# Kernel tuning notes

Measured on AMD Instinct MI355X. Metric: run time of the kernel, lower is better.

## Reference

```python
import jax, jax.numpy as jnp
import numpy as np

B, T, C, H = 2, 2048, 1024, 16
R = 32
LORA_SCALE = 0.5  # lora_alpha / r = (0.5*rank) / rank
HD = C // H


def setup_inputs() -> dict:
    key = jax.random.key(0)
    ks = jax.random.split(key, 8)
    std = 0.02
    return {
        "x": jax.random.normal(ks[0], (B, T, C), jnp.float32),
        "w_attn": jax.random.normal(ks[1], (3 * C, C), jnp.float32) * std,
        "b_attn": jnp.zeros((3 * C,), jnp.float32),
        "la_attn": jax.random.normal(ks[2], (R, C), jnp.float32) * std,
        "lb_attn": jax.random.normal(ks[3], (3 * C, R), jnp.float32) * std,
        "w_proj": jax.random.normal(ks[4], (C, C), jnp.float32) * std,
        "b_proj": jnp.zeros((C,), jnp.float32),
        "la_proj": jax.random.normal(ks[5], (R, C), jnp.float32) * std,
        "lb_proj": jax.random.normal(ks[6], (C, R), jnp.float32) * std,
    }


def lora_linear(x, w, b, la, lb):
    # y = x @ W^T + b + scale * (x @ A^T) @ B^T
    return x @ w.T + b + LORA_SCALE * ((x @ la.T) @ lb.T)


def reference(x, w_attn, b_attn, la_attn, lb_attn, w_proj, b_proj, la_proj, lb_proj):
    Bsz, Tlen, Cdim = x.shape
    qkv = lora_linear(x, w_attn, b_attn, la_attn, lb_attn)  # [B,T,3C]
    q, k, v = jnp.split(qkv, 3, axis=2)
    # [B,T,C] -> [B,H,T,hd]
    rs = lambda t: t.reshape(Bsz, Tlen, H, HD).transpose(0, 2, 1, 3)
    q, k, v = rs(q), rs(k), rs(v)
    att = jnp.einsum("bhqd,bhkd->bhqk", q, k) * (1.0 / np.sqrt(HD))
    causal = jnp.tril(jnp.ones((Tlen, Tlen), dtype=bool))
    att = jnp.where(causal[None, None], att, -jnp.inf)
    att = jax.nn.softmax(att, axis=-1)
    y = jnp.einsum("bhqk,bhkd->bhqd", att, v)  # [B,H,T,hd]
    y = y.transpose(0, 2, 1, 3).reshape(Bsz, Tlen, Cdim)
    return lora_linear(y, w_proj, b_proj, la_proj, lb_proj)
```

## Files before the change

kernel.cpp:

```cpp
#include <hip/hip_runtime.h>
#include <hip/hip_bf16.h>


typedef __attribute__((ext_vector_type(8))) short short8;
typedef __attribute__((ext_vector_type(4))) float float4v;

static __device__ __forceinline__ float b2f(ushort u) {
  union { uint i; float f; } v; v.i = ((uint)u) << 16; return v.f;
}
static __device__ __forceinline__ ushort f2b(float f) {
  union { float f; uint i; } v; v.f = f;
  uint i = v.i + 0x7fffu + ((v.i >> 16) & 1u);
  return (ushort)(i >> 16);
}
static __device__ __forceinline__ float4v zero4() {
  float4v z = {0.f, 0.f, 0.f, 0.f}; return z;
}
static __device__ __forceinline__ void glld16(const void* g, void* l) {
  __builtin_amdgcn_global_load_lds((const __attribute__((address_space(1))) void*)g,
                                   (__attribute__((address_space(3))) void*)l,
                                   16, 0, 0);
}

__global__ __launch_bounds__(256) void convert_all(
    const float* __restrict__ x, const float* __restrict__ wa,
    const float* __restrict__ la, const float* __restrict__ lb,
    const float* __restrict__ wp, const float* __restrict__ lp,
    const float* __restrict__ lq,
    ushort* __restrict__ xb, ushort* __restrict__ wab, ushort* __restrict__ lab,
    ushort* __restrict__ lbb, ushort* __restrict__ wpb, ushort* __restrict__ lpb,
    ushort* __restrict__ lqb) {
  const int stride = gridDim.x * blockDim.x;
  for (int i = blockIdx.x * blockDim.x + threadIdx.x; i < 2146304; i += stride) {
    const float* s; ushort* d; int off;
    if (i < 1048576)      { s = x;  d = xb;  off = i; }
    else if (i < 1835008) { s = wa; d = wab; off = i - 1048576; }
    else if (i < 1843200) { s = la; d = lab; off = i - 1835008; }
    else if (i < 1867776) { s = lb; d = lbb; off = i - 1843200; }
    else if (i < 2129920) { s = wp; d = wpb; off = i - 1867776; }
    else if (i < 2138112) { s = lp; d = lpb; off = i - 2129920; }
    else                  { s = lq; d = lqb; off = i - 2138112; }
    float4 v = ((const float4*)s)[off];
    union { ushort u[4]; uint2 p; } o;
    o.u[0] = f2b(v.x); o.u[1] = f2b(v.y); o.u[2] = f2b(v.z); o.u[3] = f2b(v.w);
    ((uint2*)d)[off] = o.p;
  }
}

__global__ __launch_bounds__(256) void lora_t(
    const ushort* __restrict__ X, const ushort* __restrict__ La,
    ushort* __restrict__ T) {
  const int tid = threadIdx.x;
  const int m = blockIdx.x * 8 + (tid >> 5);
  const int r = tid & 31;
  const uint4* xr = (const uint4*)(X + (size_t)m * 1024);
  const uint4* lr = (const uint4*)(La + (size_t)r * 1024);
  float s = 0.f;
#pragma unroll 4
  for (int kk = 0; kk < 128; ++kk) {
    uint4 xv = xr[kk], lv = lr[kk];
    s += b2f((ushort)xv.x) * b2f((ushort)lv.x) + b2f((ushort)(xv.x >> 16)) * b2f((ushort)(lv.x >> 16));
    s += b2f((ushort)xv.y) * b2f((ushort)lv.y) + b2f((ushort)(xv.y >> 16)) * b2f((ushort)(lv.y >> 16));
    s += b2f((ushort)xv.z) * b2f((ushort)lv.z) + b2f((ushort)(xv.z >> 16)) * b2f((ushort)(lv.z >> 16));
    s += b2f((ushort)xv.w) * b2f((ushort)lv.w) + b2f((ushort)(xv.w >> 16)) * b2f((ushort)(lv.w >> 16));
  }
  T[(size_t)m * 32 + r] = f2b(0.5f * s);
}

template <bool OUTF32, bool VSPLIT>
__global__ __launch_bounds__(256) void gemm_lora(
    const ushort* __restrict__ A, const ushort* __restrict__ W,
    const float* __restrict__ bias,
    const ushort* __restrict__ T1, const ushort* __restrict__ Lb,
    void* __restrict__ outv, ushort* __restrict__ vt, int K, int ldo) {
  __shared__ __attribute__((aligned(16))) ushort As[128 * 64];
  __shared__ __attribute__((aligned(16))) ushort Ws[128 * 64];
  const int tid = threadIdx.x;
  const int lane = tid & 63, wv = tid >> 6;
  const int l15 = lane & 15, quad = lane >> 4;
  const int m0 = blockIdx.y * 128, n0 = blockIdx.x * 128;
  const int wm = (wv >> 1) * 64, wn = (wv & 1) * 64;
  const int r8 = lane >> 3, c8 = (lane & 7) * 8;

  float4v acc[4][4];
#pragma unroll
  for (int i = 0; i < 4; i++)
#pragma unroll
    for (int j = 0; j < 4; j++) acc[i][j] = zero4();

  const int KT = K >> 6;
  for (int kt = 0; kt < KT; ++kt) {
    const int k0 = kt * 64;
    __syncthreads();
#pragma unroll
    for (int u = 0; u < 4; ++u) {
      int R = wv * 32 + u * 8;
      glld16(A + (size_t)(m0 + R + r8) * K + k0 + c8, &As[R * 64 + lane * 8]);
      glld16(W + (size_t)(n0 + R + r8) * K + k0 + c8, &Ws[R * 64 + lane * 8]);
    }
    __syncthreads();
#pragma unroll
    for (int ks = 0; ks < 2; ++ks) {
      short8 af[4], wf[4];
#pragma unroll
      for (int i = 0; i < 4; i++)
        af[i] = *(const short8*)&As[(wm + i * 16 + l15) * 64 + ks * 32 + quad * 8];
#pragma unroll
      for (int j = 0; j < 4; j++)
        wf[j] = *(const short8*)&Ws[(wn + j * 16 + l15) * 64 + ks * 32 + quad * 8];
#pragma unroll
      for (int i = 0; i < 4; i++)
#pragma unroll
        for (int j = 0; j < 4; j++)
          acc[i][j] = __builtin_amdgcn_mfma_f32_16x16x32_bf16(af[i], wf[j], acc[i][j], 0, 0, 0);
    }
  }
  __syncthreads();
#pragma unroll
  for (int c = 0; c < 2; ++c) {
    int ch = tid * 2 + c;
    int row = ch >> 2, sub = ch & 3;
    *(uint4*)&As[row * 64 + sub * 8] = *(const uint4*)(T1 + (size_t)(m0 + row) * 32 + sub * 8);
    *(uint4*)&Ws[row * 64 + sub * 8] = *(const uint4*)(Lb + (size_t)(n0 + row) * 32 + sub * 8);
  }
  __syncthreads();
  {
    short8 af[4], wf[4];
#pragma unroll
    for (int i = 0; i < 4; i++)
      af[i] = *(const short8*)&As[(wm + i * 16 + l15) * 64 + quad * 8];
#pragma unroll
    for (int j = 0; j < 4; j++)
      wf[j] = *(const short8*)&Ws[(wn + j * 16 + l15) * 64 + quad * 8];
#pragma unroll
    for (int i = 0; i < 4; i++)
#pragma unroll
      for (int j = 0; j < 4; j++)
        acc[i][j] = __builtin_amdgcn_mfma_f32_16x16x32_bf16(af[i], wf[j], acc[i][j], 0, 0, 0);
  }
#pragma unroll
  for (int i = 0; i < 4; i++) {
    int gm = m0 + wm + i * 16 + quad * 4;
#pragma unroll
    for (int j = 0; j < 4; j++) {
      int gn = n0 + wn + j * 16 + l15;
      float bb = bias[gn];
      if (VSPLIT && n0 >= 2048) {
        int vc = gn - 2048;
        int bb2 = gm >> 11, t = gm & 2047;
        ushort u0 = f2b(acc[i][j][0] + bb), u1 = f2b(acc[i][j][1] + bb);
        ushort u2 = f2b(acc[i][j][2] + bb), u3 = f2b(acc[i][j][3] + bb);
        uint2 pk; pk.x = (uint)u0 | ((uint)u1 << 16); pk.y = (uint)u2 | ((uint)u3 << 16);
        *(uint2*)(vt + ((size_t)bb2 * 1024 + vc) * 2048 + t) = pk;
      } else {
#pragma unroll
        for (int r = 0; r < 4; r++) {
          float val = acc[i][j][r] + bb;
          if (OUTF32) ((float*)outv)[(size_t)(gm + r) * ldo + gn] = val;
          else        ((ushort*)outv)[(size_t)(gm + r) * ldo + gn] = f2b(val);
        }
      }
    }
  }
}

__global__ __launch_bounds__(512) void flash_attn(
    const ushort* __restrict__ qk, const ushort* __restrict__ vt,
    ushort* __restrict__ y) {
  __shared__ __attribute__((aligned(16))) ushort Ks[2][64 * 64];
  __shared__ __attribute__((aligned(16))) ushort Vts[2][64 * 64];
  __shared__ __attribute__((aligned(16))) ushort Ps[8 * 16 * 68];
  const int tid = threadIdx.x;
  const int lane = tid & 63, wv = tid >> 6;
  const int l15 = lane & 15, quad = lane >> 4;
  const int bid = blockIdx.x;
  const int idx = bid & 255;
  const int bh = idx & 31;
  const int g = idx >> 5;
  const int qb = (bid < 256) ? (15 - g) : g;
  const int b = bh >> 4, h = bh & 15;
  const ushort* qbase = qk + (size_t)b * 2048 * 2048 + h * 64;
  const ushort* kbase = qk + (size_t)b * 2048 * 2048 + 1024 + h * 64;
  const ushort* vbase = vt + ((size_t)b * 1024 + h * 64) * 2048;
  const int r8 = lane >> 3, c8 = (lane & 7) * 8;

#pragma unroll
  for (int u = 0; u < 2; ++u) {
    int R = wv * 16 + u * 8;
    glld16(qbase + (size_t)(qb * 128 + R + r8) * 2048 + c8, &Ps[R * 64 + lane * 8]);
  }
  {
    int R = wv * 8;
    glld16(kbase + (size_t)(R + r8) * 2048 + c8, &Ks[0][R * 64 + lane * 8]);
    glld16(vbase + (size_t)(R + r8) * 2048 + c8, &Vts[0][R * 64 + lane * 8]);
  }
  __syncthreads();
  short8 aq0 = *(const short8*)&Ps[(wv * 16 + l15) * 64 + quad * 8];
  short8 aq1 = *(const short8*)&Ps[(wv * 16 + l15) * 64 + 32 + quad * 8];
  __syncthreads();

  short8 ones;
#pragma unroll
  for (int e = 0; e < 8; e++) ones[e] = (short)0x3F80;

  float4v acc[4];
#pragma unroll
  for (int jt = 0; jt < 4; jt++) acc[jt] = zero4();
  float4v lacc = zero4();
  const int last = 2 * qb + 1;
  const int qrow0 = qb * 128 + wv * 16;
  const int pB = wv * 16 * 68;

  for (int kb = 0; kb <= last; ++kb) {
    const int cur = kb & 1;
    if (kb < last) {
      const int nb = cur ^ 1;
      const int R = wv * 8;
      glld16(kbase + (size_t)((kb + 1) * 64 + R + r8) * 2048 + c8, &Ks[nb][R * 64 + lane * 8]);
      glld16(vbase + (size_t)(R + r8) * 2048 + (kb + 1) * 64 + c8, &Vts[nb][R * 64 + lane * 8]);
    }
    float4v s[4];
#pragma unroll
    for (int j = 0; j < 4; ++j) {
      short8 bk0 = *(const short8*)&Ks[cur][(j * 16 + l15) * 64 + quad * 8];
      short8 bk1 = *(const short8*)&Ks[cur][(j * 16 + l15) * 64 + 32 + quad * 8];
      s[j] = zero4();
      s[j] = __builtin_amdgcn_mfma_f32_16x16x32_bf16(aq0, bk0, s[j], 0, 0, 0);
      s[j] = __builtin_amdgcn_mfma_f32_16x16x32_bf16(aq1, bk1, s[j], 0, 0, 0);
    }
    if (kb * 64 + 63 > qrow0) {
#pragma unroll
      for (int j = 0; j < 4; ++j) {
        int key = kb * 64 + j * 16 + l15;
#pragma unroll
        for (int r = 0; r < 4; ++r)
          if (key > qrow0 + quad * 4 + r) s[j][r] = -1e30f;
      }
    }
#pragma unroll
    for (int j = 0; j < 4; ++j)
#pragma unroll
      for (int r = 0; r < 4; ++r) {
        float p = exp2f(s[j][r] * 0.18033688f);
        union { float f; uint i; } u; u.f = p;
        Ps[pB + (quad * 4 + r) * 68 + j * 16 + l15] = (ushort)(u.i >> 16);
      }
#pragma unroll
    for (int kt2 = 0; kt2 < 2; ++kt2) {
      short8 pa = *(const short8*)&Ps[pB + l15 * 68 + kt2 * 32 + quad * 8];
      lacc = __builtin_amdgcn_mfma_f32_16x16x32_bf16(pa, ones, lacc, 0, 0, 0);
#pragma unroll
      for (int jt = 0; jt < 4; ++jt) {
        short8 vb = *(const short8*)&Vts[cur][(jt * 16 + l15) * 64 + kt2 * 32 + quad * 8];
        acc[jt] = __builtin_amdgcn_mfma_f32_16x16x32_bf16(pa, vb, acc[jt], 0, 0, 0);
      }
    }
    __syncthreads();
  }
#pragma unroll
  for (int r = 0; r < 4; ++r) {
    float inv = __builtin_amdgcn_rcpf(lacc[r]);
    int t = qb * 128 + wv * 16 + quad * 4 + r;
#pragma unroll
    for (int jt = 0; jt < 4; ++jt)
      y[(size_t)(b * 2048 + t) * 1024 + h * 64 + jt * 16 + l15] = f2b(acc[jt][r] * inv);
  }
}

extern "C" void kernel_launch(void* const* d_in, const int* in_sizes, int n_in,
                              void* d_out, int out_size, void* d_ws, size_t ws_size,
                              hipStream_t stream) {
  const float* x       = (const float*)d_in[0];
  const float* w_attn  = (const float*)d_in[1];
  const float* b_attn  = (const float*)d_in[2];
  const float* la_attn = (const float*)d_in[3];
  const float* lb_attn = (const float*)d_in[4];
  const float* w_proj  = (const float*)d_in[5];
  const float* b_proj  = (const float*)d_in[6];
  const float* la_proj = (const float*)d_in[7];
  const float* lb_proj = (const float*)d_in[8];

  ushort* p = (ushort*)d_ws;
  ushort* xb   = p; p += (size_t)4096 * 1024;
  ushort* wab  = p; p += (size_t)3072 * 1024;
  ushort* lab  = p; p += (size_t)32 * 1024;
  ushort* lbb  = p; p += (size_t)3072 * 32;
  ushort* wpb  = p; p += (size_t)1024 * 1024;
  ushort* lpb  = p; p += (size_t)32 * 1024;
  ushort* lqb  = p; p += (size_t)1024 * 32;
  ushort* t1b  = p; p += (size_t)4096 * 32;
  ushort* t2b  = p; p += (size_t)4096 * 32;
  ushort* qkb  = p; p += (size_t)4096 * 2048;
  ushort* vtb  = p; p += (size_t)2048 * 2048;
  ushort* yb   = p; p += (size_t)4096 * 1024;

  convert_all<<<dim3(2048), dim3(256), 0, stream>>>(
      x, w_attn, la_attn, lb_attn, w_proj, la_proj, lb_proj,
      xb, wab, lab, lbb, wpb, lpb, lqb);
  lora_t<<<dim3(512), dim3(256), 0, stream>>>(xb, lab, t1b);
  gemm_lora<false, true><<<dim3(24, 32), dim3(256), 0, stream>>>(
      xb, wab, b_attn, t1b, lbb, qkb, vtb, 1024, 2048);
  flash_attn<<<dim3(512), dim3(512), 0, stream>>>(qkb, vtb, yb);
  lora_t<<<dim3(512), dim3(256), 0, stream>>>(yb, lpb, t2b);
  gemm_lora<true, false><<<dim3(8, 32), dim3(256), 0, stream>>>(
      yb, wpb, b_proj, t2b, lqb, d_out, nullptr, 1024, 1024);
}
```

Before: 305.0 us.

## Double-buffer GEMM LDS tiles, fold LoRA tile into pipeline, remap grid per XCD

Splits the LoRA GEMM's K loop into 32-wide tiles held in two LDS buffers. The next tile is prefetched with global_load_lds while MFMAs run on the current one, which removes one barrier per iteration and hides load latency. The LoRA low-rank update is handled as one extra pipelined K stage instead of a separate synchronous LDS fill. The launch becomes a 1D grid whose block index is remapped so that consecutive row tiles cluster per XCD, aiming for better L2 reuse. Separately, the global_load_lds LDS destinations now pass a wave-uniform base pointer; this is a correctness cleanup rather than a speed change.

```diff
diff --git a/kernel.cpp b/kernel.cpp
--- a/kernel.cpp
+++ b/kernel.cpp
@@ -67,20 +67,25 @@
   T[(size_t)m * 32 + r] = f2b(0.5f * s);
 }
 
-template <bool OUTF32, bool VSPLIT>
+template <bool OUTF32, bool VSPLIT, int NBX>
 __global__ __launch_bounds__(256) void gemm_lora(
     const ushort* __restrict__ A, const ushort* __restrict__ W,
     const float* __restrict__ bias,
     const ushort* __restrict__ T1, const ushort* __restrict__ Lb,
     void* __restrict__ outv, ushort* __restrict__ vt, int K, int ldo) {
-  __shared__ __attribute__((aligned(16))) ushort As[128 * 64];
-  __shared__ __attribute__((aligned(16))) ushort Ws[128 * 64];
+  __shared__ __attribute__((aligned(16))) ushort As[2][128 * 32];
+  __shared__ __attribute__((aligned(16))) ushort Ws[2][128 * 32];
   const int tid = threadIdx.x;
   const int lane = tid & 63, wv = tid >> 6;
   const int l15 = lane & 15, quad = lane >> 4;
-  const int m0 = blockIdx.y * 128, n0 = blockIdx.x * 128;
+  const int L = blockIdx.x;
+  const int x8 = L & 7, q = L >> 3;
+  const int bx = q % NBX;
+  const int by = x8 * 4 + q / NBX;
+  const int m0 = by * 128, n0 = bx * 128;
   const int wm = (wv >> 1) * 64, wn = (wv & 1) * 64;
-  const int r8 = lane >> 3, c8 = (lane & 7) * 8;
+  const int r4 = lane >> 2, c4 = (lane & 3) * 8;
+  const int KT = K >> 5;
 
   float4v acc[4][4];
 #pragma unroll
@@ -88,56 +93,37 @@
 #pragma unroll
     for (int j = 0; j < 4; j++) acc[i][j] = zero4();
 
-  const int KT = K >> 6;
-  for (int kt = 0; kt < KT; ++kt) {
-    const int k0 = kt * 64;
+  auto stage = [&](int t, int buf) {
+    const ushort* sA; const ushort* sW; int ld, k0;
+    if (t < KT) { sA = A; sW = W; ld = K; k0 = t * 32; }
+    else        { sA = T1; sW = Lb; ld = 32; k0 = 0; }
+#pragma unroll
+    for (int u = 0; u < 2; ++u) {
+      int R = wv * 32 + u * 16;
+      glld16(sA + (size_t)(m0 + R + r4) * ld + k0 + c4, &As[buf][R * 32]);
+      glld16(sW + (size_t)(n0 + R + r4) * ld + k0 + c4, &Ws[buf][R * 32]);
+    }
+  };
+
+  stage(0, 0);
+  for (int t = 0; t <= KT; ++t) {
     __syncthreads();
-#pragma unroll
-    for (int u = 0; u < 4; ++u) {
-      int R = wv * 32 + u * 8;
-      glld16(A + (size_t)(m0 + R + r8) * K + k0 + c8, &As[R * 64 + lane * 8]);
-      glld16(W + (size_t)(n0 + R + r8) * K + k0 + c8, &Ws[R * 64 + lane * 8]);
-    }
-    __syncthreads();
-#pragma unroll
-    for (int ks = 0; ks < 2; ++ks) {
-      short8 af[4], wf[4];
-#pragma unroll
-      for (int i = 0; i < 4; i++)
-        af[i] = *(const short8*)&As[(wm + i * 16 + l15) * 64 + ks * 32 + quad * 8];
-#pragma unroll
-      for (int j = 0; j < 4; j++)
-        wf[j] = *(const short8*)&Ws[(wn + j * 16 + l15) * 64 + ks * 32 + quad * 8];
-#pragma unroll
-      for (int i = 0; i < 4; i++)
-#pragma unroll
-        for (int j = 0; j < 4; j++)
-          acc[i][j] = __builtin_amdgcn_mfma_f32_16x16x32_bf16(af[i], wf[j], acc[i][j], 0, 0, 0);
-    }
-  }
-  __syncthreads();
-#pragma unroll
-  for (int c = 0; c < 2; ++c) {
-    int ch = tid * 2 + c;
-    int row = ch >> 2, sub = ch & 3;
-    *(uint4*)&As[row * 64 + sub * 8] = *(const uint4*)(T1 + (size_t)(m0 + row) * 32 + sub * 8);
-    *(uint4*)&Ws[row * 64 + sub * 8] = *(const uint4*)(Lb + (size_t)(n0 + row) * 32 + sub * 8);
-  }
-  __syncthreads();
-  {
+    if (t < KT) stage(t + 1, (t + 1) & 1);
+    const int b = t & 1;
     short8 af[4], wf[4];
 #pragma unroll
     for (int i = 0; i < 4; i++)
-      af[i] = *(const short8*)&As[(wm + i * 16 + l15) * 64 + quad * 8];
+      af[i] = *(const short8*)&As[b][(wm + i * 16 + l15) * 32 + quad * 8];
 #pragma unroll
     for (int j = 0; j < 4; j++)
-      wf[j] = *(const short8*)&Ws[(wn + j * 16 + l15) * 64 + quad * 8];
+      wf[j] = *(const short8*)&Ws[b][(wn + j * 16 + l15) * 32 + quad * 8];
 #pragma unroll
     for (int i = 0; i < 4; i++)
 #pragma unroll
       for (int j = 0; j < 4; j++)
         acc[i][j] = __builtin_amdgcn_mfma_f32_16x16x32_bf16(af[i], wf[j], acc[i][j], 0, 0, 0);
   }
+
 #pragma unroll
   for (int i = 0; i < 4; i++) {
     int gm = m0 + wm + i * 16 + quad * 4;
@@ -187,12 +173,12 @@
 #pragma unroll
   for (int u = 0; u < 2; ++u) {
     int R = wv * 16 + u * 8;
-    glld16(qbase + (size_t)(qb * 128 + R + r8) * 2048 + c8, &Ps[R * 64 + lane * 8]);
+    glld16(qbase + (size_t)(qb * 128 + R + r8) * 2048 + c8, &Ps[R * 64]);
   }
   {
     int R = wv * 8;
-    glld16(kbase + (size_t)(R + r8) * 2048 + c8, &Ks[0][R * 64 + lane * 8]);
-    glld16(vbase + (size_t)(R + r8) * 2048 + c8, &Vts[0][R * 64 + lane * 8]);
+    glld16(kbase + (size_t)(R + r8) * 2048 + c8, &Ks[0][R * 64]);
+    glld16(vbase + (size_t)(R + r8) * 2048 + c8, &Vts[0][R * 64]);
   }
   __syncthreads();
   short8 aq0 = *(const short8*)&Ps[(wv * 16 + l15) * 64 + quad * 8];
@@ -216,8 +202,8 @@
     if (kb < last) {
       const int nb = cur ^ 1;
       const int R = wv * 8;
-      glld16(kbase + (size_t)((kb + 1) * 64 + R + r8) * 2048 + c8, &Ks[nb][R * 64 + lane * 8]);
-      glld16(vbase + (size_t)(R + r8) * 2048 + (kb + 1) * 64 + c8, &Vts[nb][R * 64 + lane * 8]);
+      glld16(kbase + (size_t)((kb + 1) * 64 + R + r8) * 2048 + c8, &Ks[nb][R * 64]);
+      glld16(vbase + (size_t)(R + r8) * 2048 + (kb + 1) * 64 + c8, &Vts[nb][R * 64]);
     }
     float4v s[4];
 #pragma unroll
@@ -298,10 +284,10 @@
       x, w_attn, la_attn, lb_attn, w_proj, la_proj, lb_proj,
       xb, wab, lab, lbb, wpb, lpb, lqb);
   lora_t<<<dim3(512), dim3(256), 0, stream>>>(xb, lab, t1b);
-  gemm_lora<false, true><<<dim3(24, 32), dim3(256), 0, stream>>>(
+  gemm_lora<false, true, 24><<<dim3(768), dim3(256), 0, stream>>>(
       xb, wab, b_attn, t1b, lbb, qkb, vtb, 1024, 2048);
   flash_attn<<<dim3(512), dim3(512), 0, stream>>>(qkb, vtb, yb);
   lora_t<<<dim3(512), dim3(256), 0, stream>>>(yb, lpb, t2b);
-  gemm_lora<true, false><<<dim3(8, 32), dim3(256), 0, stream>>>(
+  gemm_lora<true, false, 8><<<dim3(256), dim3(256), 0, stream>>>(
       yb, wpb, b_proj, t2b, lqb, d_out, nullptr, 1024, 1024);
 }
```

After: 284.5 us. 6.7% less time.
